# Kernel optimization log

Hardware: AMD Instinct MI355X
Metric: run time of the kernel (lower is better)

The kernel has to match this reference:

```python
import jax, jax.numpy as jnp
import numpy as np

# FPN level layout for a 1024x1024 input image
LEVEL_HW = [(128, 128), (64, 64), (32, 32), (16, 16), (8, 8)]
STRIDES = [8, 16, 32, 64, 128]
IMG = 1024.0
NUM_CLASSES = 80
SCORE_THRESH = 0.2
NMS_THRESH = 0.6
TOPK = 1000
DETS = 100
BATCH = 8
TOTAL = sum(h * w for h, w in LEVEL_HW)  # 21824


def _make_anchors():
    rows = []
    for (h, w), s in zip(LEVEL_HW, STRIDES):
        xs = (np.arange(w, dtype=np.float32) + 0.5) * s
        ys = (np.arange(h, dtype=np.float32) + 0.5) * s
        xx, yy = np.meshgrid(xs, ys, indexing='ij')  # x-major, matches transpose(2,3) flatten
        pts = np.stack([xx.ravel(), yy.ravel(), xx.ravel(), yy.ravel()], axis=1)
        rows.append(pts)
    return np.concatenate(rows, axis=0).astype(np.float32)


def setup_inputs() -> dict:
    key = jax.random.key(0)
    k1, k2, k3 = jax.random.split(key, 3)
    cls_logits = jax.random.normal(k1, (BATCH, TOTAL, NUM_CLASSES), dtype=jnp.float32)
    bbox_regression = jax.random.uniform(k2, (BATCH, TOTAL, 4), dtype=jnp.float32) * 64.0
    bbox_ctrness = jax.random.normal(k3, (BATCH, TOTAL, 1), dtype=jnp.float32)
    anchors = jnp.asarray(_make_anchors())
    return {"cls_logits": cls_logits, "bbox_regression": bbox_regression,
            "bbox_ctrness": bbox_ctrness, "anchors": anchors}


def _iou_matrix(b):
    # b: [N,4] -> [N,N] pairwise IoU
    area = jnp.clip(b[:, 2] - b[:, 0], 0) * jnp.clip(b[:, 3] - b[:, 1], 0)
    lt = jnp.maximum(b[:, None, :2], b[None, :, :2])
    rb = jnp.minimum(b[:, None, 2:], b[None, :, 2:])
    wh = jnp.clip(rb - lt, 0)
    inter = wh[..., 0] * wh[..., 1]
    union = area[:, None] + area[None, :] - inter
    return inter / jnp.maximum(union, 1e-9)


def _postprocess_one(logits, reg, ctr, anchors):
    boxes_l, scores_l, labels_l = [], [], []
    off = 0
    for (h, w) in LEVEL_HW:
        n = h * w
        lg = logits[off:off + n]          # [n, C]
        rg = reg[off:off + n]             # [n, 4]
        ct = ctr[off:off + n, 0]          # [n]
        an = anchors[off:off + n]         # [n, 4]
        vals = lg.max(axis=-1)
        cls = jnp.argmax(lg, axis=-1)
        sc = jnp.sqrt(jax.nn.sigmoid(vals) * jax.nn.sigmoid(ct))
        # masked threshold + top-k  ==  filter-then-topk of the original
        masked = jnp.where(sc > SCORE_THRESH, sc, -1.0)
        k = min(TOPK, n)
        tv, ti = jax.lax.top_k(masked, k)
        a = an[ti]
        r = rg[ti]
        cx = (a[:, 0] + a[:, 2]) * 0.5
        cy = (a[:, 1] + a[:, 3]) * 0.5
        bx = jnp.stack([cx - r[:, 0], cy - r[:, 1], cx + r[:, 2], cy + r[:, 3]], axis=-1)
        bx = jnp.clip(bx, 0.0, IMG)       # clip_boxes_to_image
        boxes_l.append(bx)
        scores_l.append(tv)
        labels_l.append(cls[ti])
        off += n
    boxes = jnp.concatenate(boxes_l, axis=0)    # [N,4], N=3320
    scores = jnp.concatenate(scores_l, axis=0)  # [N]
    labels = jnp.concatenate(labels_l, axis=0)  # [N]
    N = boxes.shape[0]
    valid = scores > SCORE_THRESH
    order = jnp.argsort(-scores)
    boxes = boxes[order]
    scores = scores[order]
    labels = labels[order]
    valid = valid[order]
    # batched_nms: offset boxes per class so cross-class IoU is 0
    boff = boxes + (labels.astype(boxes.dtype) * (IMG + 1.0))[:, None]
    iou = _iou_matrix(boff)
    idx = jnp.arange(N)
    def body(i, active):
        sup = (iou[i] > NMS_THRESH) & (idx > i) & active[i]
        return active & ~sup
    active = jax.lax.fori_loop(0, N, body, valid)
    fsc = jnp.where(active, scores, -jnp.inf)
    tv, ti = jax.lax.top_k(fsc, DETS)
    m = tv > SCORE_THRESH
    out_boxes = jnp.where(m[:, None], boxes[ti], 0.0)
    out_scores = jnp.where(m, tv, 0.0)
    out_labels = jnp.where(m, labels[ti], -1)
    return out_boxes, out_scores, out_labels


def reference(cls_logits, bbox_regression, bbox_ctrness, anchors):
    fn = lambda l, r, c: _postprocess_one(l, r, c, anchors)
    boxes, scores, labels = jax.vmap(fn)(cls_logits, bbox_regression, bbox_ctrness)
    return boxes, scores, labels
```

## Files before the change

kernel.cpp:

```cpp
#include <hip/hip_runtime.h>
#include <stdint.h>

typedef unsigned long long u64;
typedef unsigned int u32;

#define BATCH   8
#define TOTAL   21824
#define NCLS    80
#define NDET    100
#define IMGSZ   1024.0f
#define STHR    0.2f
#define NMST    0.6f
#define NBUCK   4096
#define BMAX    4031
#define KGLOB   1000
#define NLOC    22
#define PRE     1024

__device__ __forceinline__ float sigm(float x) { return 1.0f / (1.0f + expf(-x)); }

__device__ __forceinline__ u32 mapKm(float s) {
    u32 u = __float_as_uint(s);
    u32 m = u ^ ((u & 0x80000000u) ? 0xFFFFFFFFu : 0x80000000u);
    return ~m;
}
__device__ __forceinline__ float unmapKm(u32 km) {
    return __uint_as_float((~km) ^ 0x80000000u);
}
__device__ __forceinline__ u64 makeKey(float s, u32 idx) {
    return (((u64)mapKm(s)) << 32) | (u64)idx;
}

__device__ __forceinline__ int bucketOfV(float s) {
    int b = (int)(__fmul_rn(__fsub_rn(1.0f, s), 5040.0f));
    return b > BMAX ? BMAX : b;
}

__device__ __forceinline__ bool suppress(float4 a, float4 c) {
    float aa = __fmul_rn(fmaxf(__fsub_rn(a.z, a.x), 0.f), fmaxf(__fsub_rn(a.w, a.y), 0.f));
    float ac = __fmul_rn(fmaxf(__fsub_rn(c.z, c.x), 0.f), fmaxf(__fsub_rn(c.w, c.y), 0.f));
    float ltx = fmaxf(a.x, c.x), lty = fmaxf(a.y, c.y);
    float rbx = fminf(a.z, c.z), rby = fminf(a.w, c.w);
    float iw = fmaxf(__fsub_rn(rbx, ltx), 0.f), ih = fmaxf(__fsub_rn(rby, lty), 0.f);
    float inter = __fmul_rn(iw, ih);
    float uni = __fsub_rn(__fadd_rn(aa, ac), inter);
    float iou = __fdiv_rn(inter, fmaxf(uni, 1e-9f));
    return iou > NMST;
}

__global__ __launch_bounds__(256) void zero_hist(u32* __restrict__ g) {
    ((uint4*)g)[blockIdx.x * 256 + threadIdx.x] = make_uint4(0u, 0u, 0u, 0u);
}

__global__ __launch_bounds__(256) void score_kernel(
        const float* __restrict__ logits, const float* __restrict__ ctr,
        float* __restrict__ mscore, int* __restrict__ mlabel,
        u32* __restrict__ ghist) {
    const int b = blockIdx.y;
    const int tid = threadIdx.x;
    const int wave = tid >> 6, lane = tid & 63;
    const int g = lane >> 2, j = lane & 3;
    const int rowBase = blockIdx.x * 256 + wave * 64;
#pragma unroll
    for (int t = 0; t < 4; t++) {
        int r = rowBase + 16 * t + g;
        bool valid = r < TOTAL;
        float best = -1e30f; int bi = 0;
        if (valid) {
            const float* rowp = logits + ((size_t)b * TOTAL + r) * NCLS + j * 4;
#pragma unroll
            for (int u = 0; u < 5; u++) {
                float4 v = *(const float4*)(rowp + u * 16);
                int c0 = u * 16 + j * 4;
                if (v.x > best) { best = v.x; bi = c0; }
                if (v.y > best) { best = v.y; bi = c0 + 1; }
                if (v.z > best) { best = v.z; bi = c0 + 2; }
                if (v.w > best) { best = v.w; bi = c0 + 3; }
            }
        }
#pragma unroll
        for (int off = 1; off <= 2; off <<= 1) {
            float ob = __shfl_xor(best, off);
            int obi = __shfl_xor(bi, off);
            if (ob > best || (ob == best && obi < bi)) { best = ob; bi = obi; }
        }
        if (valid && j == 0) {
            float c = ctr[(size_t)b * TOTAL + r];
            float sc = sqrtf(sigm(best) * sigm(c));
            bool pass = sc > STHR;
            mscore[(size_t)b * TOTAL + r] = pass ? sc : -1.0f;
            mlabel[(size_t)b * TOTAL + r] = bi;
            if (pass) atomicAdd(&ghist[(size_t)b * NBUCK + bucketOfV(sc)], 1u);
        }
    }
}

__global__ __launch_bounds__(1024) void nms_kernel(
        const float* __restrict__ mscore, const int* __restrict__ mlabel,
        const float* __restrict__ anchors, const float* __restrict__ reg,
        const u32* __restrict__ ghist, float* __restrict__ out) {
    __shared__ u32 cur[NBUCK];
    __shared__ u64 skey[2048];
    __shared__ float4 preB[PRE];
    __shared__ float4 preR[PRE];
    __shared__ int    preL[PRE];
    __shared__ u32 waveSum[16], waveOff[16];
    __shared__ u32 sh_B, sh_m;
    __shared__ int s_count;
    __shared__ float4 accB[NDET];
    __shared__ float4 accR[NDET];
    __shared__ float  accS[NDET];
    __shared__ int    accL[NDET];
    __shared__ float4 wb[64], wraw[64];
    __shared__ int    wLab[64];
    __shared__ u64 wsup[64];
    __shared__ u64 sRej[16];

    const int b = blockIdx.x, tid = threadIdx.x;
    const int wave = tid >> 6, lane = tid & 63;
    const float* ms = mscore + (size_t)b * TOTAL;
    const int* ml = mlabel + (size_t)b * TOTAL;
    const float4* anch4 = (const float4*)anchors;
    const float4* reg4 = ((const float4*)reg) + (size_t)b * TOTAL;

    uint4 hv = ((const uint4*)(ghist + (size_t)b * NBUCK))[tid];

    float sv[NLOC];
#pragma unroll
    for (int k = 0; k < NLOC; k++) {
        int i = tid + (k << 10);
        sv[k] = (i < TOTAL) ? ms[i] : -1.0f;
    }

    u32 h0 = hv.x, h1 = hv.y, h2 = hv.z, h3 = hv.w;
    u32 s = h0 + h1 + h2 + h3;
    u32 incl = s;
    for (int o = 1; o < 64; o <<= 1) {
        u32 t2 = (u32)__shfl_up((int)incl, o);
        if (lane >= o) incl += t2;
    }
    if (lane == 63) waveSum[wave] = incl;
    __syncthreads();
    if (tid == 0) {
        u32 acc = 0;
#pragma unroll
        for (int w = 0; w < 16; w++) { waveOff[w] = acc; acc += waveSum[w]; }
        sh_m = acc;
        sh_B = (u32)BMAX;
        s_count = 0;
    }
    __syncthreads();
    const u32 E = waveOff[wave] + incl - s;
    const u32 p1 = E + h0, p2 = p1 + h1, p3 = p2 + h2, p4 = p3 + h3;
    if      (E  < KGLOB && KGLOB <= p1) { sh_B = (u32)(4 * tid);     sh_m = p1; }
    else if (p1 < KGLOB && KGLOB <= p2) { sh_B = (u32)(4 * tid + 1); sh_m = p2; }
    else if (p2 < KGLOB && KGLOB <= p3) { sh_B = (u32)(4 * tid + 2); sh_m = p3; }
    else if (p3 < KGLOB && KGLOB <= p4) { sh_B = (u32)(4 * tid + 3); sh_m = p4; }
    cur[4 * tid]     = E;
    cur[4 * tid + 1] = p1;
    cur[4 * tid + 2] = p2;
    cur[4 * tid + 3] = p3;
    __syncthreads();
    const int Bstar = (int)sh_B;

#pragma unroll
    for (int k = 0; k < NLOC; k++) {
        float s0 = sv[k];
        if (s0 > STHR) {
            int bk = bucketOfV(s0);
            if (bk <= Bstar) {
                int pos = (int)atomicAdd(&cur[bk], 1u);
                if (pos < 2048) skey[pos] = makeKey(s0, (u32)(tid + (k << 10)));
            }
        }
    }
    __syncthreads();

#pragma unroll
    for (int q = 0; q < 4; q++) {
        int bk = 4 * tid + q;
        u32 cnt = (q == 0) ? h0 : (q == 1) ? h1 : (q == 2) ? h2 : h3;
        u32 lo0 = (q == 0) ? E  : (q == 1) ? p1 : (q == 2) ? p2 : p3;
        if (bk <= Bstar && cnt > 1) {
            int lo = (int)lo0;
            int hi = lo + (int)cnt; if (hi > 2048) hi = 2048;
            for (int i2 = lo + 1; i2 < hi; i2++) {
                u64 key = skey[i2];
                int j2 = i2 - 1;
                while (j2 >= lo && skey[j2] > key) { skey[j2 + 1] = skey[j2]; j2--; }
                skey[j2 + 1] = key;
            }
        }
    }
    __syncthreads();
    int m = (int)sh_m; if (m > 2048) m = 2048;
    const int Pm = m < PRE ? m : PRE;

    for (int p = tid; p < Pm; p += 1024) {
        u64 key = skey[p];
        int idx = (int)(key & 0xFFFFFFFFu);
        float4 a = anch4[idx];
        float4 r = reg4[idx];
        int lb = ml[idx];
        float cx = (a.x + a.z) * 0.5f;
        float cy = (a.y + a.w) * 0.5f;
        float x1 = fminf(fmaxf(cx - r.x, 0.0f), IMGSZ);
        float y1 = fminf(fmaxf(cy - r.y, 0.0f), IMGSZ);
        float x2 = fminf(fmaxf(cx + r.z, 0.0f), IMGSZ);
        float y2 = fminf(fmaxf(cy + r.w, 0.0f), IMGSZ);
        float off = (float)lb * (IMGSZ + 1.0f);
        preR[p] = make_float4(x1, y1, x2, y2);
        preB[p] = make_float4(__fadd_rn(x1, off), __fadd_rn(y1, off),
                              __fadd_rn(x2, off), __fadd_rn(y2, off));
        preL[p] = lb;
    }
    __syncthreads();

    int count = 0, Ew = 0;
    while (true) {
        int take = m - Ew; if (take > 64) take = 64;
        if (take <= 0) break;
        const bool ldsPath = (Ew + take <= Pm);

        if (!ldsPath) {
            if (tid < take) {
                int idx = (int)(skey[Ew + tid] & 0xFFFFFFFFu);
                float4 a = anch4[idx];
                float4 r = reg4[idx];
                int lb = ml[idx];
                float cx = (a.x + a.z) * 0.5f;
                float cy = (a.y + a.w) * 0.5f;
                float x1 = fminf(fmaxf(cx - r.x, 0.0f), IMGSZ);
                float y1 = fminf(fmaxf(cy - r.y, 0.0f), IMGSZ);
                float x2 = fminf(fmaxf(cx + r.z, 0.0f), IMGSZ);
                float y2 = fminf(fmaxf(cy + r.w, 0.0f), IMGSZ);
                float off = (float)lb * (IMGSZ + 1.0f);
                wraw[tid] = make_float4(x1, y1, x2, y2);
                wb[tid] = make_float4(__fadd_rn(x1, off), __fadd_rn(y1, off),
                                      __fadd_rn(x2, off), __fadd_rn(y2, off));
                wLab[tid] = lb;
            }
            __syncthreads();
        }

        {
            float4 myB;
            if (lane < take) myB = ldsPath ? preB[Ew + lane] : wb[lane];
            bool rej = false;
            if (lane < take) {
                for (int s2 = wave; s2 < count; s2 += 16) {
                    if (suppress(accB[s2], myB)) { rej = true; break; }
                }
            }
            u64 mask = __ballot(rej);
            if (lane == 0) sRej[wave] = mask;
            for (int rr = wave; rr < take; rr += 16) {
                float4 rB = ldsPath ? preB[Ew + rr] : wb[rr];
                bool sp = (lane < take && lane > rr) ? suppress(rB, myB) : false;
                u64 msk = __ballot(sp);
                if (lane == 0) wsup[rr] = msk;
            }
        }
        __syncthreads();

        if (wave == 0) {
            u64 rj = (lane < 16) ? sRej[lane] : 0ull;
#pragma unroll
            for (int o = 1; o < 64; o <<= 1) rj |= __shfl_xor(rj, o);
            u64 supr = (lane < take) ? wsup[lane] : 0ull;
            u64 validb = (take >= 64) ? ~0ull : ((1ull << take) - 1ull);
            u64 aliveM = validb & ~rj;
            u64 contrib = ((aliveM >> lane) & 1ull) ? supr : 0ull;
            u64 U = contrib;
#pragma unroll
            for (int o = 1; o < 64; o <<= 1) U |= __shfl_xor(U, o);
            int space = NDET - count;
            u64 accM;
            if ((U & aliveM) == 0ull) {
                accM = aliveM;
            } else {
                u64 rem = aliveM; accM = 0ull;
                while (rem) {
                    int rr = __builtin_ctzll(rem);
                    accM |= 1ull << rr;
                    if (__popcll(accM) >= space) break;
                    u64 sr = __shfl(supr, rr);
                    rem &= ~(1ull << rr);
                    rem &= ~sr;
                }
            }
            int na = __popcll(accM);
            int takeA = na < space ? na : space;
            if (lane < take && ((accM >> lane) & 1ull)) {
                int pos = __popcll(accM & ((1ull << lane) - 1ull));
                if (pos < takeA) {
                    int o2 = count + pos;
                    accB[o2] = ldsPath ? preB[Ew + lane] : wb[lane];
                    accR[o2] = ldsPath ? preR[Ew + lane] : wraw[lane];
                    accL[o2] = ldsPath ? preL[Ew + lane] : wLab[lane];
                    accS[o2] = unmapKm((u32)(skey[Ew + lane] >> 32));
                }
            }
            if (lane == 0) s_count = count + takeA;
        }
        __syncthreads();
        count = s_count;
        Ew += take;
        if (count >= NDET) break;
    }
    __syncthreads();

    for (int s2 = tid; s2 < NDET; s2 += 1024) {
        float4 bxv = make_float4(0.f, 0.f, 0.f, 0.f);
        float scv = 0.0f, lbv = -1.0f;
        if (s2 < count) {
            bxv = accR[s2];
            scv = accS[s2];
            lbv = (float)accL[s2];
        }
        ((float4*)out)[b * NDET + s2] = bxv;
        out[BATCH * NDET * 4 + b * NDET + s2] = scv;
        out[BATCH * NDET * 4 + BATCH * NDET + b * NDET + s2] = lbv;
    }
}

extern "C" void kernel_launch(void* const* d_in, const int* in_sizes, int n_in,
                              void* d_out, int out_size, void* d_ws, size_t ws_size,
                              hipStream_t stream) {
    (void)in_sizes; (void)n_in; (void)out_size; (void)ws_size;
    const float* logits  = (const float*)d_in[0];
    const float* reg     = (const float*)d_in[1];
    const float* ctr     = (const float*)d_in[2];
    const float* anchors = (const float*)d_in[3];
    float* out = (float*)d_out;

    char* ws = (char*)d_ws;
    size_t off = 0;
    auto alloc = [&](size_t bytes) -> void* {
        off = (off + 255) & ~(size_t)255;
        void* p = ws + off;
        off += bytes;
        return p;
    };
    float* mscore = (float*)alloc((size_t)BATCH * TOTAL * 4);
    int*   mlabel = (int*)  alloc((size_t)BATCH * TOTAL * 4);
    u32*   ghist  = (u32*)  alloc((size_t)BATCH * NBUCK * 4);

    zero_hist<<<dim3((BATCH * NBUCK) / (256 * 4)), 256, 0, stream>>>(ghist);
    score_kernel<<<dim3((TOTAL + 255) / 256, BATCH), 256, 0, stream>>>(logits, ctr, mscore, mlabel, ghist);
    nms_kernel<<<BATCH, 1024, 0, stream>>>(mscore, mlabel, anchors, reg, ghist, out);
}
```

Measured before the change: 133.0 us.

## Fuse score and NMS kernels using last-block-done ticket per batch

Merges the scoring kernel and the per-image NMS kernel into one launch. Each 1024-thread block scores 256 rows, then bumps a per-batch counter, and the last block to arrive for that image runs histogram selection, sorting and NMS. Shared memory is cut by reusing the bucket cursor array as preR and by fetching labels from global memory at output time instead of staging them. This removes one kernel launch and its gap, but the NMS tail now starts in whichever block finishes last, and the larger 1024-thread blocks with heavy LDS use may lower score-phase occupancy.

After: 166.0 us. 24.8% more time.

```diff
diff --git a/kernel.cpp b/kernel.cpp
--- a/kernel.cpp
+++ b/kernel.cpp
@@ -16,6 +16,9 @@
 #define KGLOB   1000
 #define NLOC    22
 #define PRE     1024
+#define NBLK    86
+#define DSTRIDE 8
+#define ZN      ((BATCH * NBUCK + 64) / 4)
 
 __device__ __forceinline__ float sigm(float x) { return 1.0f / (1.0f + expf(-x)); }
 
@@ -49,21 +52,36 @@
 }
 
 __global__ __launch_bounds__(256) void zero_hist(u32* __restrict__ g) {
-    ((uint4*)g)[blockIdx.x * 256 + threadIdx.x] = make_uint4(0u, 0u, 0u, 0u);
-}
-
-__global__ __launch_bounds__(256) void score_kernel(
+    int i = blockIdx.x * 256 + threadIdx.x;
+    if (i < ZN) ((uint4*)g)[i] = make_uint4(0u, 0u, 0u, 0u);
+}
+
+__global__ __launch_bounds__(1024) void fused_kernel(
         const float* __restrict__ logits, const float* __restrict__ ctr,
+        const float* __restrict__ reg, const float* __restrict__ anchors,
         float* __restrict__ mscore, int* __restrict__ mlabel,
-        u32* __restrict__ ghist) {
-    const int b = blockIdx.y;
-    const int tid = threadIdx.x;
+        u32* __restrict__ ghist, u32* __restrict__ done,
+        float* __restrict__ out) {
+    __shared__ u64 skey[2048];
+    __shared__ float4 preB[PRE];
+    __shared__ u32 curbuf[NBUCK];
+    __shared__ u32 waveSum[16], waveOff[16];
+    __shared__ u32 sh_B, sh_m;
+    __shared__ int s_count, sh_ticket;
+    __shared__ float4 accB[NDET];
+    __shared__ float4 accR[NDET];
+    __shared__ float  accS[NDET];
+    __shared__ int    accIdx[NDET];
+    __shared__ float4 wb[64], wraw[64];
+    __shared__ u64 wsup[64];
+    __shared__ u64 sRej[16];
+
+    const int b = blockIdx.y, tid = threadIdx.x;
     const int wave = tid >> 6, lane = tid & 63;
     const int g = lane >> 2, j = lane & 3;
-    const int rowBase = blockIdx.x * 256 + wave * 64;
-#pragma unroll
-    for (int t = 0; t < 4; t++) {
-        int r = rowBase + 16 * t + g;
+
+    {
+        int r = blockIdx.x * 256 + wave * 16 + g;
         bool valid = r < TOTAL;
         float best = -1e30f; int bi = 0;
         if (valid) {
@@ -93,31 +111,16 @@
             if (pass) atomicAdd(&ghist[(size_t)b * NBUCK + bucketOfV(sc)], 1u);
         }
     }
-}
-
-__global__ __launch_bounds__(1024) void nms_kernel(
-        const float* __restrict__ mscore, const int* __restrict__ mlabel,
-        const float* __restrict__ anchors, const float* __restrict__ reg,
-        const u32* __restrict__ ghist, float* __restrict__ out) {
-    __shared__ u32 cur[NBUCK];
-    __shared__ u64 skey[2048];
-    __shared__ float4 preB[PRE];
-    __shared__ float4 preR[PRE];
-    __shared__ int    preL[PRE];
-    __shared__ u32 waveSum[16], waveOff[16];
-    __shared__ u32 sh_B, sh_m;
-    __shared__ int s_count;
-    __shared__ float4 accB[NDET];
-    __shared__ float4 accR[NDET];
-    __shared__ float  accS[NDET];
-    __shared__ int    accL[NDET];
-    __shared__ float4 wb[64], wraw[64];
-    __shared__ int    wLab[64];
-    __shared__ u64 wsup[64];
-    __shared__ u64 sRej[16];
-
-    const int b = blockIdx.x, tid = threadIdx.x;
-    const int wave = tid >> 6, lane = tid & 63;
+
+    __syncthreads();
+    if (tid == 0) {
+        __threadfence();
+        sh_ticket = (int)atomicAdd(&done[(size_t)b * DSTRIDE], 1u);
+    }
+    __syncthreads();
+    if (sh_ticket != NBLK - 1) return;
+    __threadfence();
+
     const float* ms = mscore + (size_t)b * TOTAL;
     const int* ml = mlabel + (size_t)b * TOTAL;
     const float4* anch4 = (const float4*)anchors;
@@ -156,10 +159,10 @@
     else if (p1 < KGLOB && KGLOB <= p2) { sh_B = (u32)(4 * tid + 1); sh_m = p2; }
     else if (p2 < KGLOB && KGLOB <= p3) { sh_B = (u32)(4 * tid + 2); sh_m = p3; }
     else if (p3 < KGLOB && KGLOB <= p4) { sh_B = (u32)(4 * tid + 3); sh_m = p4; }
-    cur[4 * tid]     = E;
-    cur[4 * tid + 1] = p1;
-    cur[4 * tid + 2] = p2;
-    cur[4 * tid + 3] = p3;
+    curbuf[4 * tid]     = E;
+    curbuf[4 * tid + 1] = p1;
+    curbuf[4 * tid + 2] = p2;
+    curbuf[4 * tid + 3] = p3;
     __syncthreads();
     const int Bstar = (int)sh_B;
 
@@ -169,12 +172,13 @@
         if (s0 > STHR) {
             int bk = bucketOfV(s0);
             if (bk <= Bstar) {
-                int pos = (int)atomicAdd(&cur[bk], 1u);
+                int pos = (int)atomicAdd(&curbuf[bk], 1u);
                 if (pos < 2048) skey[pos] = makeKey(s0, (u32)(tid + (k << 10)));
             }
         }
     }
     __syncthreads();
+    float4* preR = (float4*)curbuf;
 
 #pragma unroll
     for (int q = 0; q < 4; q++) {
@@ -212,7 +216,6 @@
         preR[p] = make_float4(x1, y1, x2, y2);
         preB[p] = make_float4(__fadd_rn(x1, off), __fadd_rn(y1, off),
                               __fadd_rn(x2, off), __fadd_rn(y2, off));
-        preL[p] = lb;
     }
     __syncthreads();
 
@@ -238,7 +241,6 @@
                 wraw[tid] = make_float4(x1, y1, x2, y2);
                 wb[tid] = make_float4(__fadd_rn(x1, off), __fadd_rn(y1, off),
                                       __fadd_rn(x2, off), __fadd_rn(y2, off));
-                wLab[tid] = lb;
             }
             __syncthreads();
         }
@@ -295,10 +297,11 @@
                 int pos = __popcll(accM & ((1ull << lane) - 1ull));
                 if (pos < takeA) {
                     int o2 = count + pos;
+                    u64 key = skey[Ew + lane];
                     accB[o2] = ldsPath ? preB[Ew + lane] : wb[lane];
                     accR[o2] = ldsPath ? preR[Ew + lane] : wraw[lane];
-                    accL[o2] = ldsPath ? preL[Ew + lane] : wLab[lane];
-                    accS[o2] = unmapKm((u32)(skey[Ew + lane] >> 32));
+                    accIdx[o2] = (int)(key & 0xFFFFFFFFu);
+                    accS[o2] = unmapKm((u32)(key >> 32));
                 }
             }
             if (lane == 0) s_count = count + takeA;
@@ -316,7 +319,7 @@
         if (s2 < count) {
             bxv = accR[s2];
             scv = accS[s2];
-            lbv = (float)accL[s2];
+            lbv = (float)ml[accIdx[s2]];
         }
         ((float4*)out)[b * NDET + s2] = bxv;
         out[BATCH * NDET * 4 + b * NDET + s2] = scv;
@@ -344,9 +347,10 @@
     };
     float* mscore = (float*)alloc((size_t)BATCH * TOTAL * 4);
     int*   mlabel = (int*)  alloc((size_t)BATCH * TOTAL * 4);
-    u32*   ghist  = (u32*)  alloc((size_t)BATCH * NBUCK * 4);
-
-    zero_hist<<<dim3((BATCH * NBUCK) / (256 * 4)), 256, 0, stream>>>(ghist);
-    score_kernel<<<dim3((TOTAL + 255) / 256, BATCH), 256, 0, stream>>>(logits, ctr, mscore, mlabel, ghist);
-    nms_kernel<<<BATCH, 1024, 0, stream>>>(mscore, mlabel, anchors, reg, ghist, out);
-}
+    u32*   ghist  = (u32*)  alloc((size_t)(BATCH * NBUCK + 64) * 4);
+    u32*   done   = ghist + (size_t)BATCH * NBUCK;
+
+    zero_hist<<<dim3((ZN + 255) / 256), 256, 0, stream>>>(ghist);
+    fused_kernel<<<dim3(NBLK, BATCH), 1024, 0, stream>>>(
+        logits, ctr, reg, anchors, mscore, mlabel, ghist, done, out);
+}
```

## Defer argmax to NMS candidates, refine candidate buckets, batch logit loads

Applied to the files above, without the earlier changes.

The score kernel now computes only the max logit, loads all four rows' logits up front, and no longer writes a per-anchor label array. The NMS kernel recomputes the argmax label only for the roughly 1000 preselected candidates by rereading their logit rows. It also re-buckets candidates with a finer key-based histogram so the per-bucket insertion sorts run on smaller groups, and reuses that shared buffer as preR to save LDS. The cost is an extra prefix scan and extra syncs in the single-block-per-image NMS kernel, plus scattered 320-byte logit row reads there.

After: 127.0 us. 4.5% less time.

```diff
diff --git a/kernel.cpp b/kernel.cpp
--- a/kernel.cpp
+++ b/kernel.cpp
@@ -16,6 +16,7 @@
 #define KGLOB   1000
 #define NLOC    22
 #define PRE     1024
+#define ZN      ((BATCH * NBUCK) / 4)
 
 __device__ __forceinline__ float sigm(float x) { return 1.0f / (1.0f + expf(-x)); }
 
@@ -49,61 +50,85 @@
 }
 
 __global__ __launch_bounds__(256) void zero_hist(u32* __restrict__ g) {
-    ((uint4*)g)[blockIdx.x * 256 + threadIdx.x] = make_uint4(0u, 0u, 0u, 0u);
+    int i = blockIdx.x * 256 + threadIdx.x;
+    if (i < ZN) ((uint4*)g)[i] = make_uint4(0u, 0u, 0u, 0u);
 }
 
 __global__ __launch_bounds__(256) void score_kernel(
         const float* __restrict__ logits, const float* __restrict__ ctr,
-        float* __restrict__ mscore, int* __restrict__ mlabel,
-        u32* __restrict__ ghist) {
+        float* __restrict__ mscore, u32* __restrict__ ghist) {
     const int b = blockIdx.y;
     const int tid = threadIdx.x;
     const int wave = tid >> 6, lane = tid & 63;
     const int g = lane >> 2, j = lane & 3;
     const int rowBase = blockIdx.x * 256 + wave * 64;
+
+    int r[4]; bool valid[4];
 #pragma unroll
     for (int t = 0; t < 4; t++) {
-        int r = rowBase + 16 * t + g;
-        bool valid = r < TOTAL;
-        float best = -1e30f; int bi = 0;
-        if (valid) {
-            const float* rowp = logits + ((size_t)b * TOTAL + r) * NCLS + j * 4;
-#pragma unroll
-            for (int u = 0; u < 5; u++) {
-                float4 v = *(const float4*)(rowp + u * 16);
-                int c0 = u * 16 + j * 4;
-                if (v.x > best) { best = v.x; bi = c0; }
-                if (v.y > best) { best = v.y; bi = c0 + 1; }
-                if (v.z > best) { best = v.z; bi = c0 + 2; }
-                if (v.w > best) { best = v.w; bi = c0 + 3; }
-            }
-        }
-#pragma unroll
-        for (int off = 1; off <= 2; off <<= 1) {
-            float ob = __shfl_xor(best, off);
-            int obi = __shfl_xor(bi, off);
-            if (ob > best || (ob == best && obi < bi)) { best = ob; bi = obi; }
-        }
-        if (valid && j == 0) {
-            float c = ctr[(size_t)b * TOTAL + r];
-            float sc = sqrtf(sigm(best) * sigm(c));
+        int rr = rowBase + 16 * t + g;
+        valid[t] = rr < TOTAL;
+        r[t] = valid[t] ? rr : (TOTAL - 1);
+    }
+    float4 vv[20]; float cc[4];
+#pragma unroll
+    for (int t = 0; t < 4; t++) {
+        const float* rowp = logits + ((size_t)b * TOTAL + r[t]) * NCLS + j * 4;
+#pragma unroll
+        for (int u = 0; u < 5; u++)
+            vv[t * 5 + u] = *(const float4*)(rowp + u * 16);
+    }
+#pragma unroll
+    for (int t = 0; t < 4; t++) cc[t] = ctr[(size_t)b * TOTAL + r[t]];
+
+#pragma unroll
+    for (int t = 0; t < 4; t++) {
+        float m0 = -1e30f;
+#pragma unroll
+        for (int u = 0; u < 5; u++) {
+            float4 v = vv[t * 5 + u];
+            m0 = fmaxf(m0, fmaxf(fmaxf(v.x, v.y), fmaxf(v.z, v.w)));
+        }
+        m0 = fmaxf(m0, __shfl_xor(m0, 1));
+        m0 = fmaxf(m0, __shfl_xor(m0, 2));
+        if (valid[t] && j == 0) {
+            float sc = sqrtf(sigm(m0) * sigm(cc[t]));
             bool pass = sc > STHR;
-            mscore[(size_t)b * TOTAL + r] = pass ? sc : -1.0f;
-            mlabel[(size_t)b * TOTAL + r] = bi;
+            mscore[(size_t)b * TOTAL + r[t]] = pass ? sc : -1.0f;
             if (pass) atomicAdd(&ghist[(size_t)b * NBUCK + bucketOfV(sc)], 1u);
         }
     }
 }
 
+__device__ __forceinline__ int rowLabel(const float4* __restrict__ row4) {
+    float best = -1e30f;
+#pragma unroll
+    for (int k = 0; k < 20; k++) {
+        float4 q = row4[k];
+        best = fmaxf(best, fmaxf(fmaxf(q.x, q.y), fmaxf(q.z, q.w)));
+    }
+    int lb = -1;
+#pragma unroll
+    for (int k = 0; k < 20; k++) {
+        float4 q = row4[k];
+        if (lb < 0) {
+            if      (q.x == best) lb = 4 * k;
+            else if (q.y == best) lb = 4 * k + 1;
+            else if (q.z == best) lb = 4 * k + 2;
+            else if (q.w == best) lb = 4 * k + 3;
+        }
+    }
+    return lb;
+}
+
 __global__ __launch_bounds__(1024) void nms_kernel(
-        const float* __restrict__ mscore, const int* __restrict__ mlabel,
+        const float* __restrict__ mscore, const float* __restrict__ logits,
         const float* __restrict__ anchors, const float* __restrict__ reg,
         const u32* __restrict__ ghist, float* __restrict__ out) {
-    __shared__ u32 cur[NBUCK];
     __shared__ u64 skey[2048];
     __shared__ float4 preB[PRE];
-    __shared__ float4 preR[PRE];
-    __shared__ int    preL[PRE];
+    __shared__ u32 curbuf[NBUCK];
+    __shared__ int preL[PRE];
     __shared__ u32 waveSum[16], waveOff[16];
     __shared__ u32 sh_B, sh_m;
     __shared__ int s_count;
@@ -119,9 +144,9 @@
     const int b = blockIdx.x, tid = threadIdx.x;
     const int wave = tid >> 6, lane = tid & 63;
     const float* ms = mscore + (size_t)b * TOTAL;
-    const int* ml = mlabel + (size_t)b * TOTAL;
     const float4* anch4 = (const float4*)anchors;
     const float4* reg4 = ((const float4*)reg) + (size_t)b * TOTAL;
+    const float* lg = logits + (size_t)b * TOTAL * NCLS;
 
     uint4 hv = ((const uint4*)(ghist + (size_t)b * NBUCK))[tid];
 
@@ -150,38 +175,79 @@
         s_count = 0;
     }
     __syncthreads();
-    const u32 E = waveOff[wave] + incl - s;
-    const u32 p1 = E + h0, p2 = p1 + h1, p3 = p2 + h2, p4 = p3 + h3;
-    if      (E  < KGLOB && KGLOB <= p1) { sh_B = (u32)(4 * tid);     sh_m = p1; }
-    else if (p1 < KGLOB && KGLOB <= p2) { sh_B = (u32)(4 * tid + 1); sh_m = p2; }
-    else if (p2 < KGLOB && KGLOB <= p3) { sh_B = (u32)(4 * tid + 2); sh_m = p3; }
-    else if (p3 < KGLOB && KGLOB <= p4) { sh_B = (u32)(4 * tid + 3); sh_m = p4; }
-    cur[4 * tid]     = E;
-    cur[4 * tid + 1] = p1;
-    cur[4 * tid + 2] = p2;
-    cur[4 * tid + 3] = p3;
+    {
+        const u32 E = waveOff[wave] + incl - s;
+        const u32 p1 = E + h0, p2 = p1 + h1, p3 = p2 + h2, p4 = p3 + h3;
+        if      (E  < KGLOB && KGLOB <= p1) { sh_B = (u32)(4 * tid);     sh_m = p1; }
+        else if (p1 < KGLOB && KGLOB <= p2) { sh_B = (u32)(4 * tid + 1); sh_m = p2; }
+        else if (p2 < KGLOB && KGLOB <= p3) { sh_B = (u32)(4 * tid + 2); sh_m = p3; }
+        else if (p3 < KGLOB && KGLOB <= p4) { sh_B = (u32)(4 * tid + 3); sh_m = p4; }
+    }
+    curbuf[tid] = 0; curbuf[tid + 1024] = 0; curbuf[tid + 2048] = 0; curbuf[tid + 3072] = 0;
     __syncthreads();
     const int Bstar = (int)sh_B;
+
+    const float sLo = 1.0f - (float)(Bstar + 2) * (1.0f / 5040.0f);
+    const u32 kmMin = mapKm(1.0f);
+    const u32 kmMax = mapKm(sLo);
+    const u32 range = kmMax - kmMin + 1u;
+    int hib = 32 - __clz(range);
+    const int fsh = hib > 12 ? hib - 12 : 0;
 
 #pragma unroll
     for (int k = 0; k < NLOC; k++) {
         float s0 = sv[k];
-        if (s0 > STHR) {
-            int bk = bucketOfV(s0);
-            if (bk <= Bstar) {
-                int pos = (int)atomicAdd(&cur[bk], 1u);
-                if (pos < 2048) skey[pos] = makeKey(s0, (u32)(tid + (k << 10)));
-            }
-        }
-    }
-    __syncthreads();
+        if (s0 > STHR && bucketOfV(s0) <= Bstar) {
+            u32 fb = (mapKm(s0) - kmMin) >> fsh;
+            if (fb > 4095u) fb = 4095u;
+            atomicAdd(&curbuf[fb], 1u);
+        }
+    }
+    __syncthreads();
+
+    u32 f0 = curbuf[4 * tid], f1 = curbuf[4 * tid + 1],
+        f2 = curbuf[4 * tid + 2], f3 = curbuf[4 * tid + 3];
+    u32 fs = f0 + f1 + f2 + f3;
+    u32 fincl = fs;
+    for (int o = 1; o < 64; o <<= 1) {
+        u32 t2 = (u32)__shfl_up((int)fincl, o);
+        if (lane >= o) fincl += t2;
+    }
+    __syncthreads();
+    if (lane == 63) waveSum[wave] = fincl;
+    __syncthreads();
+    if (tid == 0) {
+        u32 acc = 0;
+#pragma unroll
+        for (int w = 0; w < 16; w++) { waveOff[w] = acc; acc += waveSum[w]; }
+    }
+    __syncthreads();
+    const u32 E2 = waveOff[wave] + fincl - fs;
+    const u32 q1 = E2 + f0, q2 = q1 + f1, q3 = q2 + f2;
+    curbuf[4 * tid]     = E2;
+    curbuf[4 * tid + 1] = q1;
+    curbuf[4 * tid + 2] = q2;
+    curbuf[4 * tid + 3] = q3;
+    __syncthreads();
+
+#pragma unroll
+    for (int k = 0; k < NLOC; k++) {
+        float s0 = sv[k];
+        if (s0 > STHR && bucketOfV(s0) <= Bstar) {
+            u32 fb = (mapKm(s0) - kmMin) >> fsh;
+            if (fb > 4095u) fb = 4095u;
+            int pos = (int)atomicAdd(&curbuf[fb], 1u);
+            if (pos < 2048) skey[pos] = makeKey(s0, (u32)(tid + (k << 10)));
+        }
+    }
+    __syncthreads();
+    float4* preR = (float4*)curbuf;
 
 #pragma unroll
     for (int q = 0; q < 4; q++) {
-        int bk = 4 * tid + q;
-        u32 cnt = (q == 0) ? h0 : (q == 1) ? h1 : (q == 2) ? h2 : h3;
-        u32 lo0 = (q == 0) ? E  : (q == 1) ? p1 : (q == 2) ? p2 : p3;
-        if (bk <= Bstar && cnt > 1) {
+        u32 cnt = (q == 0) ? f0 : (q == 1) ? f1 : (q == 2) ? f2 : f3;
+        u32 lo0 = (q == 0) ? E2 : (q == 1) ? q1 : (q == 2) ? q2 : q3;
+        if (cnt > 1) {
             int lo = (int)lo0;
             int hi = lo + (int)cnt; if (hi > 2048) hi = 2048;
             for (int i2 = lo + 1; i2 < hi; i2++) {
@@ -201,7 +267,7 @@
         int idx = (int)(key & 0xFFFFFFFFu);
         float4 a = anch4[idx];
         float4 r = reg4[idx];
-        int lb = ml[idx];
+        int lb = rowLabel((const float4*)(lg + (size_t)idx * NCLS));
         float cx = (a.x + a.z) * 0.5f;
         float cy = (a.y + a.w) * 0.5f;
         float x1 = fminf(fmaxf(cx - r.x, 0.0f), IMGSZ);
@@ -227,7 +293,7 @@
                 int idx = (int)(skey[Ew + tid] & 0xFFFFFFFFu);
                 float4 a = anch4[idx];
                 float4 r = reg4[idx];
-                int lb = ml[idx];
+                int lb = rowLabel((const float4*)(lg + (size_t)idx * NCLS));
                 float cx = (a.x + a.z) * 0.5f;
                 float cy = (a.y + a.w) * 0.5f;
                 float x1 = fminf(fmaxf(cx - r.x, 0.0f), IMGSZ);
@@ -295,10 +361,11 @@
                 int pos = __popcll(accM & ((1ull << lane) - 1ull));
                 if (pos < takeA) {
                     int o2 = count + pos;
+                    u64 key = skey[Ew + lane];
                     accB[o2] = ldsPath ? preB[Ew + lane] : wb[lane];
                     accR[o2] = ldsPath ? preR[Ew + lane] : wraw[lane];
                     accL[o2] = ldsPath ? preL[Ew + lane] : wLab[lane];
-                    accS[o2] = unmapKm((u32)(skey[Ew + lane] >> 32));
+                    accS[o2] = unmapKm((u32)(key >> 32));
                 }
             }
             if (lane == 0) s_count = count + takeA;
@@ -343,10 +410,9 @@
         return p;
     };
     float* mscore = (float*)alloc((size_t)BATCH * TOTAL * 4);
-    int*   mlabel = (int*)  alloc((size_t)BATCH * TOTAL * 4);
     u32*   ghist  = (u32*)  alloc((size_t)BATCH * NBUCK * 4);
 
-    zero_hist<<<dim3((BATCH * NBUCK) / (256 * 4)), 256, 0, stream>>>(ghist);
-    score_kernel<<<dim3((TOTAL + 255) / 256, BATCH), 256, 0, stream>>>(logits, ctr, mscore, mlabel, ghist);
-    nms_kernel<<<BATCH, 1024, 0, stream>>>(mscore, mlabel, anchors, reg, ghist, out);
-}
+    zero_hist<<<dim3((ZN + 255) / 256), 256, 0, stream>>>(ghist);
+    score_kernel<<<dim3((TOTAL + 255) / 256, BATCH), 256, 0, stream>>>(logits, ctr, mscore, ghist);
+    nms_kernel<<<BATCH, 1024, 0, stream>>>(mscore, logits, anchors, reg, ghist, out);
+}
```
